# Performance work log

Measured on AMD Instinct MI355X. Metric: run time of the kernel, lower is better.

## Reference

```python
import jax, jax.numpy as jnp
import numpy as np

B, S, H = 2, 2048, 4096
NH, NKV, HD = 32, 8, 128
BASE = 10000.0


def setup_inputs() -> dict:
    key = jax.random.key(0)
    ks = jax.random.split(key, 5)
    sc = 0.02
    hidden_states = jax.random.normal(ks[0], (B, S, H), dtype=jnp.float32)
    position_ids = jnp.broadcast_to(jnp.arange(S, dtype=jnp.int64)[None, :], (B, S))
    Wq = jax.random.normal(ks[1], (H, NH * HD), dtype=jnp.float32) * sc
    Wk = jax.random.normal(ks[2], (H, NKV * HD), dtype=jnp.float32) * sc
    Wv = jax.random.normal(ks[3], (H, NKV * HD), dtype=jnp.float32) * sc
    Wo = jax.random.normal(ks[4], (NH * HD, H), dtype=jnp.float32) * sc
    return {"hidden_states": hidden_states, "position_ids": position_ids,
            "Wq": Wq, "Wk": Wk, "Wv": Wv, "Wo": Wo}


def _rotate_half(x):
    x1, x2 = x[..., : x.shape[-1] // 2], x[..., x.shape[-1] // 2:]
    return jnp.concatenate((-x2, x1), axis=-1)


def _rope_tables(position_ids, head_dim):
    inv_freq = 1.0 / (BASE ** (jnp.arange(0, head_dim, 2, dtype=jnp.float32) / head_dim))
    # freqs per gathered position: [B, S, HD/2] -> emb [B, S, HD]
    freqs = position_ids.astype(jnp.float32)[..., None] * inv_freq
    emb = jnp.concatenate((freqs, freqs), axis=-1)
    # add head axis: [B, 1, S, HD]
    return jnp.cos(emb)[:, None, :, :], jnp.sin(emb)[:, None, :, :]


def reference(hidden_states, position_ids, Wq, Wk, Wv, Wo):
    b, s, _ = hidden_states.shape
    q = (hidden_states @ Wq).reshape(b, s, NH, HD).transpose(0, 2, 1, 3)   # [B,NH,S,HD]
    k = (hidden_states @ Wk).reshape(b, s, NKV, HD).transpose(0, 2, 1, 3)  # [B,NKV,S,HD]
    v = (hidden_states @ Wv).reshape(b, s, NKV, HD).transpose(0, 2, 1, 3)

    cos, sin = _rope_tables(position_ids, HD)
    q = q * cos + _rotate_half(q) * sin
    k = k * cos + _rotate_half(k) * sin

    # GQA repeat_kv
    n_rep = NH // NKV
    k = jnp.repeat(k, n_rep, axis=1)  # [B,NH,S,HD]
    v = jnp.repeat(v, n_rep, axis=1)

    scores = jnp.einsum('bhqd,bhkd->bhqk', q, k) / jnp.sqrt(jnp.float32(HD))
    causal = jnp.tril(jnp.ones((s, s), dtype=bool))
    scores = jnp.where(causal[None, None], scores, jnp.finfo(scores.dtype).min)
    attn = jax.nn.softmax(scores, axis=-1)

    out = jnp.einsum('bhqk,bhkd->bhqd', attn, v)          # [B,NH,S,HD]
    out = out.transpose(0, 2, 1, 3).reshape(b, s, NH * HD)
    return out @ Wo
```

## Files before the change

kernel.cpp:

```cpp
#include <hip/hip_runtime.h>
#include <stdint.h>
#include <math.h>

#define Bn   2
#define Sn   2048
#define Hn   4096
#define NHn  32
#define NKVn 8
#define HDn  128
#define Mn   (Bn*Sn)
#define NQKVn 6144

typedef unsigned short u16;
typedef __attribute__((ext_vector_type(8))) short  short8;
typedef __attribute__((ext_vector_type(4))) float  f32x4;

__device__ __forceinline__ u16 f2b(float f){
  union{float f; uint32_t u;} v; v.f=f;
  return (u16)((v.u + 0x7fffu + ((v.u>>16)&1u))>>16);
}
__device__ __forceinline__ float b2f(u16 h){
  union{uint32_t u; float f;} v; v.u=((uint32_t)h)<<16; return v.f;
}

__device__ __forceinline__ void async_copy16(u16* lds, const u16* g){
  __builtin_amdgcn_global_load_lds((const __attribute__((address_space(1))) void*)g,
                                   (__attribute__((address_space(3))) void*)lds,
                                   16, 0, 0);
}

__global__ void cast_f32_bf16(const float* __restrict__ x, u16* __restrict__ y, int n){
  int i = (blockIdx.x*256 + threadIdx.x)*4;
  if (i < n){
    float4 v = *(const float4*)(x + i);
    ushort4 o; o.x=f2b(v.x); o.y=f2b(v.y); o.z=f2b(v.z); o.w=f2b(v.w);
    *(ushort4*)(y + i) = o;
  }
}

__global__ void transpose_cast(const float* __restrict__ w, u16* __restrict__ wt,
                               int K, int N){
  __shared__ float tile[32][33];
  int n0 = blockIdx.x*32, k0 = blockIdx.y*32;
  int t = threadIdx.x;
#pragma unroll
  for (int i=0;i<4;i++){
    int idx = t + 256*i; int lr = idx>>5, lc = idx&31;
    tile[lr][lc] = w[(size_t)(k0+lr)*N + n0 + lc];
  }
  __syncthreads();
#pragma unroll
  for (int i=0;i<4;i++){
    int idx = t + 256*i; int orr = idx>>5, oc = idx&31;
    wt[(size_t)(n0+orr)*K + k0 + oc] = f2b(tile[oc][orr]);
  }
}

__global__ void transpose_v(const u16* __restrict__ qkv, u16* __restrict__ vt){
  __shared__ u16 tile[32][33];
  int b = blockIdx.z;
  int s0 = blockIdx.x*32, d0 = blockIdx.y*32;
  int t = threadIdx.x;
#pragma unroll
  for (int i=0;i<4;i++){
    int idx = t + 256*i; int lr = idx>>5, lc = idx&31;
    tile[lr][lc] = qkv[(size_t)(b*Sn + s0 + lr)*NQKVn + 5120 + d0 + lc];
  }
  __syncthreads();
#pragma unroll
  for (int i=0;i<4;i++){
    int idx = t + 256*i; int orr = idx>>5, oc = idx&31;
    vt[((size_t)b*1024 + d0 + orr)*Sn + s0 + oc] = tile[oc][orr];
  }
}

__global__ void rope_kernel(u16* __restrict__ qkv){
  int tx = blockIdx.x*256 + threadIdx.x;
  int m  = blockIdx.y;
  int h  = tx>>6, i = tx&63;
  int col = (h < NHn) ? h*HDn + i : Hn + (h-NHn)*HDn + i;
  int pos = m & (Sn-1);
  float inv_freq = exp2f(-(float)i * 0.20762050593046015f);
  float th = (float)pos * inv_freq;
  float c, s;
  sincosf(th, &s, &c);
  size_t base = (size_t)m*NQKVn + col;
  float x1 = b2f(qkv[base]);
  float x2 = b2f(qkv[base+64]);
  qkv[base]     = f2b(x1*c - x2*s);
  qkv[base+64]  = f2b(x2*c + x1*s);
}

template<bool OUT_BF16>
__global__ __launch_bounds__(256) void gemm_bt(const u16* __restrict__ A,
                                               const u16* __restrict__ Bt,
                                               void* __restrict__ Cout,
                                               int Mdim, int Ndim, int Kdim){
  __shared__ u16 As[128*32];
  __shared__ u16 Bs[128*32];
  int m0 = blockIdx.y*128, n0 = blockIdx.x*128;
  int t = threadIdx.x;
  int w = t>>6, l = t&63;
  int lane15 = l&15, quad = l>>4;
  int wrow = (w>>1)*64, wcol = (w&1)*64;
  f32x4 acc[4][4];
#pragma unroll
  for (int mi=0;mi<4;mi++)
#pragma unroll
    for (int ni=0;ni<4;ni++) acc[mi][ni] = (f32x4){0.f,0.f,0.f,0.f};

  int kTiles = Kdim >> 5;
  for (int kt=0; kt<kTiles; kt++){
    int k0 = kt<<5;
    __syncthreads();
#pragma unroll
    for (int c=0;c<2;c++){
      int idx  = t + c*256;
      int row  = idx>>2, col8 = (idx&3)*8;
      int idx0 = (t & ~63) + c*256;
      async_copy16(&As[(size_t)idx0*8], &A [(size_t)(m0+row)*Kdim + k0 + col8]);
      async_copy16(&Bs[(size_t)idx0*8], &Bt[(size_t)(n0+row)*Kdim + k0 + col8]);
    }
    __syncthreads();
    short8 a[4], b[4];
#pragma unroll
    for (int mi=0;mi<4;mi++)
      a[mi] = *(const short8*)(&As[(wrow + mi*16 + lane15)*32 + quad*8]);
#pragma unroll
    for (int ni=0;ni<4;ni++)
      b[ni] = *(const short8*)(&Bs[(wcol + ni*16 + lane15)*32 + quad*8]);
#pragma unroll
    for (int mi=0;mi<4;mi++)
#pragma unroll
      for (int ni=0;ni<4;ni++)
        acc[mi][ni] = __builtin_amdgcn_mfma_f32_16x16x32_bf16(a[mi], b[ni], acc[mi][ni], 0,0,0);
  }
#pragma unroll
  for (int mi=0;mi<4;mi++)
#pragma unroll
    for (int ni=0;ni<4;ni++)
#pragma unroll
      for (int r=0;r<4;r++){
        int row = m0 + wrow + mi*16 + quad*4 + r;
        int col = n0 + wcol + ni*16 + lane15;
        float v = acc[mi][ni][r];
        if (OUT_BF16) ((u16*)Cout)[(size_t)row*Ndim + col] = f2b(v);
        else        ((float*)Cout)[(size_t)row*Ndim + col] = v;
      }
}

#define KSP 136

__device__ __forceinline__ void softmax_rg(
    f32x4 sacc[4], f32x4 oacc[8], float& mrun, float& lsum,
    int baserow , int j, int lane15, int quad,
    u16* myP, float sc)
{
  int qr = baserow + lane15;
  if (j*64 + 63 > baserow){
#pragma unroll
    for (int ni=0;ni<4;ni++)
#pragma unroll
      for (int r=0;r<4;r++){
        int ka = j*64 + ni*16 + quad*4 + r;
        if (ka > qr) sacc[ni][r] = -INFINITY;
      }
  }
  float mx = -INFINITY;
#pragma unroll
  for (int ni=0;ni<4;ni++)
    mx = fmaxf(mx, fmaxf(fmaxf(sacc[ni][0], sacc[ni][1]),
                         fmaxf(sacc[ni][2], sacc[ni][3])));
  mx = fmaxf(mx, __shfl_xor(mx, 16));
  mx = fmaxf(mx, __shfl_xor(mx, 32));
  float pmax = mx * sc;

  if (__any(pmax > mrun + 8.f)){
    float mnew = fmaxf(mrun, pmax);
    float alpha = exp2f(mrun - mnew);
    mrun = mnew;
    float a0 = __shfl(alpha, quad*4 + 0);
    float a1 = __shfl(alpha, quad*4 + 1);
    float a2 = __shfl(alpha, quad*4 + 2);
    float a3 = __shfl(alpha, quad*4 + 3);
#pragma unroll
    for (int ni=0;ni<8;ni++){
      oacc[ni][0] *= a0; oacc[ni][1] *= a1;
      oacc[ni][2] *= a2; oacc[ni][3] *= a3;
    }
    lsum *= alpha;
  }

  float psum = 0.f;
#pragma unroll
  for (int ni=0;ni<4;ni++){
#pragma unroll
    for (int r=0;r<4;r++)
      sacc[ni][r] = exp2f(fmaf(sacc[ni][r], sc, -mrun));
    psum += (sacc[ni][0] + sacc[ni][1]) + (sacc[ni][2] + sacc[ni][3]);
  }
  psum += __shfl_xor(psum, 16);
  psum += __shfl_xor(psum, 32);
  lsum += psum;

  uint32_t* myP32 = (uint32_t*)myP;
#pragma unroll
  for (int ni=0;ni<4;ni++)
#pragma unroll
    for (int rp=0;rp<2;rp++){
      uint32_t pk;
      asm("v_cvt_pk_bf16_f32 %0, %1, %2"
          : "=v"(pk) : "v"(sacc[ni][2*rp]), "v"(sacc[ni][2*rp+1]));
      myP32[lane15*36 + ni*8 + quad*2 + rp] = pk;
    }
}

__device__ __forceinline__ void epilogue_rg(
    f32x4 oacc[8], float lsum, u16* scr, u16* __restrict__ ob,
    size_t gbase , int l, int lane15, int quad)
{
  float inv = 1.0f / lsum;
  float i0 = __shfl(inv, quad*4 + 0);
  float i1 = __shfl(inv, quad*4 + 1);
  float i2 = __shfl(inv, quad*4 + 2);
  float i3 = __shfl(inv, quad*4 + 3);
#pragma unroll
  for (int ni=0;ni<8;ni++){
    scr[(quad*4+0)*136 + ni*16 + lane15] = f2b(oacc[ni][0]*i0);
    scr[(quad*4+1)*136 + ni*16 + lane15] = f2b(oacc[ni][1]*i1);
    scr[(quad*4+2)*136 + ni*16 + lane15] = f2b(oacc[ni][2]*i2);
    scr[(quad*4+3)*136 + ni*16 + lane15] = f2b(oacc[ni][3]*i3);
  }
  int rr = l>>2, cc = l&3;
#pragma unroll
  for (int c=0;c<4;c++){
    short8 v = *(const short8*)(&scr[rr*136 + c*32 + cc*8]);
    *(short8*)(&ob[gbase + (size_t)rr*Hn + c*32 + cc*8]) = v;
  }
}

__global__ __launch_bounds__(512, 2) void attn_kernel(const u16* __restrict__ qkv,
                                                      const u16* __restrict__ vt,
                                                      u16* __restrict__ ob){
  __shared__ u16 Ks[64*KSP];
  __shared__ u16 Vs[128*72];
  __shared__ u16 Ps[8][2][16*72];
  int bh = blockIdx.y;
  int b = bh >> 5, h = bh & 31;
  int hkv = h >> 2;
  int t = threadIdx.x, w = t>>6, l = t&63;
  int lane15 = l&15, quad = l>>4;

  const float sc = 0.08838834764831845f * 1.44269504088896340736f;
  size_t kgbase = (size_t)b*Sn*NQKVn + Hn + hkv*HDn;
  size_t vgbase = ((size_t)b*1024 + hkv*HDn)*Sn;

  for (int pass=0; pass<2; ++pass){
    int qi = pass ? (7 - (int)blockIdx.x) : (int)blockIdx.x;
    int q0 = qi*256;
    int wbase = q0 + w*32;

    short8 qf0[4], qf1[4];
    {
      size_t qb0 = (size_t)(b*Sn + wbase + lane15)*NQKVn + h*HDn;
      size_t qb1 = (size_t)(b*Sn + wbase + 16 + lane15)*NQKVn + h*HDn;
#pragma unroll
      for (int ks=0;ks<4;ks++){
        qf0[ks] = *(const short8*)(&qkv[qb0 + ks*32 + quad*8]);
        qf1[ks] = *(const short8*)(&qkv[qb1 + ks*32 + quad*8]);
      }
    }

    float mrun0 = -INFINITY, lsum0 = 0.f;
    float mrun1 = -INFINITY, lsum1 = 0.f;
    f32x4 oacc0[8], oacc1[8];
#pragma unroll
    for (int ni=0;ni<8;ni++){
      oacc0[ni] = (f32x4){0.f,0.f,0.f,0.f};
      oacc1[ni] = (f32x4){0.f,0.f,0.f,0.f};
    }

    const int nj = 4*qi + 4;

    uint4 kr[2], vr[2];
#pragma unroll
    for (int c=0;c<2;c++){
      int idx = t + 512*c;
      kr[c] = *(const uint4*)(&qkv[kgbase + (size_t)(0*64 + (idx>>4))*NQKVn + (idx&15)*8]);
      vr[c] = *(const uint4*)(&vt [vgbase + (size_t)(idx>>3)*Sn + 0*64 + (idx&7)*8]);
    }
#pragma unroll
    for (int c=0;c<2;c++){
      int idx = t + 512*c;
      *(uint4*)(&Ks[(idx>>4)*KSP + (idx&15)*8]) = kr[c];
      *(uint4*)(&Vs[(idx>>3)*72  + (idx&7)*8])  = vr[c];
    }
    __syncthreads();

    for (int j=0; j<nj; j++){
      if (j+1 < nj){
#pragma unroll
        for (int c=0;c<2;c++){
          int idx = t + 512*c;
          kr[c] = *(const uint4*)(&qkv[kgbase + (size_t)((j+1)*64 + (idx>>4))*NQKVn + (idx&15)*8]);
          vr[c] = *(const uint4*)(&vt [vgbase + (size_t)(idx>>3)*Sn + (j+1)*64 + (idx&7)*8]);
        }
      }

      bool active = (j*64) <= (wbase + 31);
      if (active){
        f32x4 s0[4], s1[4];
#pragma unroll
        for (int ni=0;ni<4;ni++){
          s0[ni] = (f32x4){0.f,0.f,0.f,0.f};
          s1[ni] = (f32x4){0.f,0.f,0.f,0.f};
        }
        __builtin_amdgcn_s_setprio(1);
#pragma unroll
        for (int ks=0;ks<4;ks++){
#pragma unroll
          for (int ni=0;ni<4;ni++){
            short8 kf = *(const short8*)(&Ks[(ni*16 + lane15)*KSP + ks*32 + quad*8]);
            s0[ni] = __builtin_amdgcn_mfma_f32_16x16x32_bf16(kf, qf0[ks], s0[ni], 0,0,0);
            s1[ni] = __builtin_amdgcn_mfma_f32_16x16x32_bf16(kf, qf1[ks], s1[ni], 0,0,0);
          }
        }
        __builtin_amdgcn_s_setprio(0);

        softmax_rg(s0, oacc0, mrun0, lsum0, wbase,      j, lane15, quad, &Ps[w][0][0], sc);
        softmax_rg(s1, oacc1, mrun1, lsum1, wbase + 16, j, lane15, quad, &Ps[w][1][0], sc);

        u16* P0 = &Ps[w][0][0];
        u16* P1 = &Ps[w][1][0];
        __builtin_amdgcn_s_setprio(1);
#pragma unroll
        for (int ks=0;ks<2;ks++){
          short8 pa0 = *(const short8*)(&P0[lane15*72 + ks*32 + quad*8]);
          short8 pa1 = *(const short8*)(&P1[lane15*72 + ks*32 + quad*8]);
#pragma unroll
          for (int ni=0;ni<8;ni++){
            short8 vb = *(const short8*)(&Vs[(ni*16 + lane15)*72 + ks*32 + quad*8]);
            oacc0[ni] = __builtin_amdgcn_mfma_f32_16x16x32_bf16(pa0, vb, oacc0[ni], 0,0,0);
            oacc1[ni] = __builtin_amdgcn_mfma_f32_16x16x32_bf16(pa1, vb, oacc1[ni], 0,0,0);
          }
        }
        __builtin_amdgcn_s_setprio(0);
      }

      __syncthreads();
      if (j+1 < nj){
#pragma unroll
        for (int c=0;c<2;c++){
          int idx = t + 512*c;
          *(uint4*)(&Ks[(idx>>4)*KSP + (idx&15)*8]) = kr[c];
          *(uint4*)(&Vs[(idx>>3)*72  + (idx&7)*8])  = vr[c];
        }
        __syncthreads();
      }
    }

    u16* scr = (w < 4) ? &Ks[w*2176] : &Vs[(w-4)*2176];
    size_t gb0 = (size_t)(b*Sn + wbase)*Hn + h*HDn;
    epilogue_rg(oacc0, lsum0, scr, ob, gb0,                    l, lane15, quad);
    epilogue_rg(oacc1, lsum1, scr, ob, gb0 + (size_t)16*Hn,    l, lane15, quad);

    __syncthreads();
  }
}

extern "C" void kernel_launch(void* const* d_in, const int* in_sizes, int n_in,
                              void* d_out, int out_size, void* d_ws, size_t ws_size,
                              hipStream_t stream){
  const float* X  = (const float*)d_in[0];
  const float* Wq = (const float*)d_in[2];
  const float* Wk = (const float*)d_in[3];
  const float* Wv = (const float*)d_in[4];
  const float* Wo = (const float*)d_in[5];
  float* out = (float*)d_out;

  char* ws = (char*)d_ws;
  const size_t MB = 1024ull*1024ull;
  u16* Xb   = (u16*)(ws);
  u16* Wt   = (u16*)(ws + 32*MB);
  u16* Wot  = (u16*)(ws + 80*MB);
  u16* QKV  = (u16*)(ws + 112*MB);
  u16* Ob   = Xb;
  u16* Vt   = Wt;

  cast_f32_bf16<<<(Mn*Hn)/4/256, 256, 0, stream>>>(X, Xb, Mn*Hn);
  transpose_cast<<<dim3(Hn/32,       Hn/32), 256, 0, stream>>>(Wq, Wt,                    Hn, Hn);
  transpose_cast<<<dim3(NKVn*HDn/32, Hn/32), 256, 0, stream>>>(Wk, Wt + (size_t)Hn*Hn,    Hn, NKVn*HDn);
  transpose_cast<<<dim3(NKVn*HDn/32, Hn/32), 256, 0, stream>>>(Wv, Wt + (size_t)5120*Hn,  Hn, NKVn*HDn);
  transpose_cast<<<dim3(Hn/32,       Hn/32), 256, 0, stream>>>(Wo, Wot,                   Hn, Hn);
  gemm_bt<true><<<dim3(NQKVn/128, Mn/128), 256, 0, stream>>>(Xb, Wt, QKV, Mn, NQKVn, Hn);
  rope_kernel<<<dim3(10, Mn), 256, 0, stream>>>(QKV);
  transpose_v<<<dim3(Sn/32, 1024/32, Bn), 256, 0, stream>>>(QKV, Vt);
  attn_kernel<<<dim3(Sn/512, Bn*NHn), 512, 0, stream>>>(QKV, Vt, Ob);
  gemm_bt<false><<<dim3(Hn/128, Mn/128), 256, 0, stream>>>(Ob, Wot, out, Mn, Hn, Hn);
}
```

Measured before the change: 895.7 us.

## Replace GEMM with 256x256-tile kernel using 4-slot async LDS pipeline and swizzle

```diff
diff --git a/kernel.cpp b/kernel.cpp
--- a/kernel.cpp
+++ b/kernel.cpp
@@ -92,57 +92,97 @@
 }
 
 template<bool OUT_BF16>
-__global__ __launch_bounds__(256) void gemm_bt(const u16* __restrict__ A,
-                                               const u16* __restrict__ Bt,
-                                               void* __restrict__ Cout,
-                                               int Mdim, int Ndim, int Kdim){
-  __shared__ u16 As[128*32];
-  __shared__ u16 Bs[128*32];
-  int m0 = blockIdx.y*128, n0 = blockIdx.x*128;
-  int t = threadIdx.x;
-  int w = t>>6, l = t&63;
+__global__ __launch_bounds__(512, 2) void gemm256(const u16* __restrict__ A,
+                                                  const u16* __restrict__ Bt,
+                                                  void* __restrict__ Cout,
+                                                  int Mdim, int Ndim, int Kdim){
+  __shared__ u16 lds[4][2][256*32];
+  int lin = blockIdx.y*gridDim.x + blockIdx.x;
+  int nwg = gridDim.x*gridDim.y;
+  int swz = (lin&7)*(nwg>>3) + (lin>>3);
+  int bx = swz % gridDim.x, by = swz / gridDim.x;
+  int m0 = by*256, n0 = bx*256;
+  int t = threadIdx.x, w = t>>6, l = t&63;
   int lane15 = l&15, quad = l>>4;
-  int wrow = (w>>1)*64, wcol = (w&1)*64;
-  f32x4 acc[4][4];
-#pragma unroll
-  for (int mi=0;mi<4;mi++)
+  int wm = w>>2, wn = w&3;
+
+  f32x4 acc[8][4];
+#pragma unroll
+  for (int mi=0;mi<8;mi++)
 #pragma unroll
     for (int ni=0;ni<4;ni++) acc[mi][ni] = (f32x4){0.f,0.f,0.f,0.f};
 
-  int kTiles = Kdim >> 5;
-  for (int kt=0; kt<kTiles; kt++){
-    int k0 = kt<<5;
-    __syncthreads();
-#pragma unroll
-    for (int c=0;c<2;c++){
-      int idx  = t + c*256;
-      int row  = idx>>2, col8 = (idx&3)*8;
-      int idx0 = (t & ~63) + c*256;
-      async_copy16(&As[(size_t)idx0*8], &A [(size_t)(m0+row)*Kdim + k0 + col8]);
-      async_copy16(&Bs[(size_t)idx0*8], &Bt[(size_t)(n0+row)*Kdim + k0 + col8]);
-    }
-    __syncthreads();
-    short8 a[4], b[4];
+  const int nst = Kdim >> 5;
+  int srow = w*16 + (l>>2);
+  int scol = ((l&3) ^ ((l>>2)&3)) << 3;
+  auto STAGE = [&](int s){
+    int slot = s&3; int k0 = s<<5;
+    const u16* ga = A  + (size_t)(m0 + srow)*Kdim + k0 + scol;
+    const u16* gb = Bt + (size_t)(n0 + srow)*Kdim + k0 + scol;
+    u16* la = &lds[slot][0][(w*16)*32];
+    u16* lb = &lds[slot][1][(w*16)*32];
+    async_copy16(la,          ga);
+    async_copy16(la + 128*32, ga + (size_t)128*Kdim);
+    async_copy16(lb,          gb);
+    async_copy16(lb + 128*32, gb + (size_t)128*Kdim);
+  };
+
+  STAGE(0); STAGE(1);
+  asm volatile("s_waitcnt vmcnt(4)" ::: "memory");
+  __builtin_amdgcn_sched_barrier(0);
+  __builtin_amdgcn_s_barrier();
+  __builtin_amdgcn_sched_barrier(0);
+
+  int rsw = (quad ^ (lane15&3)) << 3;
+  for (int s=0; s<nst; ++s){
+    if (s+2 < nst) STAGE(s+2);
+    const u16* Asl = &lds[s&3][0][0];
+    const u16* Bsl = &lds[s&3][1][0];
+    short8 bfr[4], afr[4], afr2[4];
+#pragma unroll
+    for (int ni=0;ni<4;ni++)
+      bfr[ni] = *(const short8*)(&Bsl[(wn*64 + ni*16 + lane15)*32 + rsw]);
 #pragma unroll
     for (int mi=0;mi<4;mi++)
-      a[mi] = *(const short8*)(&As[(wrow + mi*16 + lane15)*32 + quad*8]);
+      afr[mi] = *(const short8*)(&Asl[(wm*128 + mi*16 + lane15)*32 + rsw]);
+    asm volatile("s_waitcnt lgkmcnt(0)" ::: "memory");
+    __builtin_amdgcn_sched_barrier(0);
+    __builtin_amdgcn_s_setprio(1);
+#pragma unroll
+    for (int mi=0;mi<4;mi++)
+#pragma unroll
+      for (int ni=0;ni<4;ni++)
+        acc[mi][ni] = __builtin_amdgcn_mfma_f32_16x16x32_bf16(afr[mi], bfr[ni], acc[mi][ni], 0,0,0);
+    __builtin_amdgcn_s_setprio(0);
+#pragma unroll
+    for (int mi=0;mi<4;mi++)
+      afr2[mi] = *(const short8*)(&Asl[(wm*128 + (mi+4)*16 + lane15)*32 + rsw]);
+    asm volatile("s_waitcnt lgkmcnt(0)" ::: "memory");
+    __builtin_amdgcn_sched_barrier(0);
+    __builtin_amdgcn_s_setprio(1);
+#pragma unroll
+    for (int mi=0;mi<4;mi++)
+#pragma unroll
+      for (int ni=0;ni<4;ni++)
+        acc[mi+4][ni] = __builtin_amdgcn_mfma_f32_16x16x32_bf16(afr2[mi], bfr[ni], acc[mi+4][ni], 0,0,0);
+    __builtin_amdgcn_s_setprio(0);
+    if (s+1 < nst){
+      if (s+2 < nst) asm volatile("s_waitcnt vmcnt(4)" ::: "memory");
+      else           asm volatile("s_waitcnt vmcnt(0)" ::: "memory");
+      __builtin_amdgcn_sched_barrier(0);
+      __builtin_amdgcn_s_barrier();
+      __builtin_amdgcn_sched_barrier(0);
+    }
+  }
+
+#pragma unroll
+  for (int mi=0;mi<8;mi++)
 #pragma unroll
     for (int ni=0;ni<4;ni++)
-      b[ni] = *(const short8*)(&Bs[(wcol + ni*16 + lane15)*32 + quad*8]);
-#pragma unroll
-    for (int mi=0;mi<4;mi++)
-#pragma unroll
-      for (int ni=0;ni<4;ni++)
-        acc[mi][ni] = __builtin_amdgcn_mfma_f32_16x16x32_bf16(a[mi], b[ni], acc[mi][ni], 0,0,0);
-  }
-#pragma unroll
-  for (int mi=0;mi<4;mi++)
-#pragma unroll
-    for (int ni=0;ni<4;ni++)
 #pragma unroll
       for (int r=0;r<4;r++){
-        int row = m0 + wrow + mi*16 + quad*4 + r;
-        int col = n0 + wcol + ni*16 + lane15;
+        int row = m0 + wm*128 + mi*16 + quad*4 + r;
+        int col = n0 + wn*64 + ni*16 + lane15;
         float v = acc[mi][ni][r];
         if (OUT_BF16) ((u16*)Cout)[(size_t)row*Ndim + col] = f2b(v);
         else        ((float*)Cout)[(size_t)row*Ndim + col] = v;
@@ -392,9 +432,9 @@
   transpose_cast<<<dim3(NKVn*HDn/32, Hn/32), 256, 0, stream>>>(Wk, Wt + (size_t)Hn*Hn,    Hn, NKVn*HDn);
   transpose_cast<<<dim3(NKVn*HDn/32, Hn/32), 256, 0, stream>>>(Wv, Wt + (size_t)5120*Hn,  Hn, NKVn*HDn);
   transpose_cast<<<dim3(Hn/32,       Hn/32), 256, 0, stream>>>(Wo, Wot,                   Hn, Hn);
-  gemm_bt<true><<<dim3(NQKVn/128, Mn/128), 256, 0, stream>>>(Xb, Wt, QKV, Mn, NQKVn, Hn);
+  gemm256<true><<<dim3(NQKVn/256, Mn/256), 512, 0, stream>>>(Xb, Wt, QKV, Mn, NQKVn, Hn);
   rope_kernel<<<dim3(10, Mn), 256, 0, stream>>>(QKV);
   transpose_v<<<dim3(Sn/32, 1024/32, Bn), 256, 0, stream>>>(QKV, Vt);
   attn_kernel<<<dim3(Sn/512, Bn*NHn), 512, 0, stream>>>(QKV, Vt, Ob);
-  gemm_bt<false><<<dim3(Hn/128, Mn/128), 256, 0, stream>>>(Ob, Wot, out, Mn, Hn, Hn);
-}
+  gemm256<false><<<dim3(Hn/256, Mn/256), 512, 0, stream>>>(Ob, Wot, out, Mn, Hn, Hn);
+}
```

After: 814.8 us. 1.1x faster.
